# Kernel optimization log

Hardware: AMD Instinct MI355X
Metric: run time of the kernel (lower is better)

The kernel has to match this reference:

```python
import jax, jax.numpy as jnp
import numpy as np

B, H, W, C = 8, 64, 64, 256
CB = C // 2          # bottleneck_dim = channels // 2
COMPRESSION = 2      # max-pool factor on flattened spatial axis of phi and g


def setup_inputs() -> dict:
    key = jax.random.key(0)
    k = jax.random.split(key, 5)
    he = lambda kk, fan_in, shape: jax.random.normal(kk, shape, jnp.float32) * np.sqrt(2.0 / fan_in)
    return {
        "x": jax.random.normal(k[0], (B, H, W, C), jnp.float32),
        "W_theta": he(k[1], C, (C, CB)),
        "W_phi": he(k[2], C, (C, CB)),
        "W_g": he(k[3], C, (C, CB)),
        "W_out": he(k[4], CB, (CB, C)),
    }


def _maxpool1d(t, pool):
    # MaxPool1D(pool) along axis 1 of [B, N, C] (valid padding, stride=pool)
    b, n, c = t.shape
    return t.reshape(b, n // pool, pool, c).max(axis=2)


def reference(x, W_theta, W_phi, W_g, W_out):
    b, h, w, c = x.shape
    n = h * w
    xf = x.reshape(b, n, c)                      # flatten spatial dims
    theta = xf @ W_theta                         # [B, N, Cb] (1x1 conv, no bias)
    phi = _maxpool1d(xf @ W_phi, COMPRESSION)    # [B, N/2, Cb]
    g = _maxpool1d(xf @ W_g, COMPRESSION)        # [B, N/2, Cb]
    f = jax.nn.softmax(jnp.einsum('bnd,bmd->bnm', theta, phi), axis=-1)  # [B, N, N/2]
    y = jnp.einsum('bnm,bmd->bnd', f, g)         # [B, N, Cb]
    y = (y @ W_out).reshape(b, h, w, c)          # expand conv back to C
    return x + y                                 # add_residual=True
```

## Files before the change

### kernel.cpp

```cpp
#include <hip/hip_runtime.h>
#include <math.h>

#define BB 8
#define NN 4096
#define MM 2048
#define CC 256
#define CBD 128

typedef __attribute__((ext_vector_type(8))) short s16x8;
typedef __attribute__((ext_vector_type(8))) _Float16 f16x8;
typedef __attribute__((ext_vector_type(4))) float f32x4;
typedef __attribute__((ext_vector_type(16))) float f32x16;
typedef unsigned short u16;
typedef unsigned int u32;

__device__ __forceinline__ u16 f2bf(float f) {
    union { float f; u32 u; } v; v.f = f;
    u32 r = v.u + 0x7fffu + ((v.u >> 16) & 1u);
    return (u16)(r >> 16);
}
__device__ __forceinline__ float bf2f(u16 h) {
    union { u32 u; float f; } v; v.u = ((u32)h) << 16; return v.f;
}
__device__ __forceinline__ u16 f2h(float f) {
    union { _Float16 h; u16 u; } v; v.h = (_Float16)f; return v.u;
}
__device__ __forceinline__ u32 asu(float f) {
    union { float f; u32 u; } v; v.f = f; return v.u;
}
__device__ __forceinline__ u32 pkbf(float lo, float hi) {
    return __builtin_amdgcn_perm(asu(hi), asu(lo), 0x07060302u);
}

#define MFMA(a, b, c)    __builtin_amdgcn_mfma_f32_16x16x32_bf16(a, b, c, 0, 0, 0)
#define MFMAF(a, b, c)   __builtin_amdgcn_mfma_f32_16x16x32_f16(a, b, c, 0, 0, 0)
#define MFMA32(a, b, c)  __builtin_amdgcn_mfma_f32_32x32x16_bf16(a, b, c, 0, 0, 0)
#define MFMA32F(a, b, c) __builtin_amdgcn_mfma_f32_32x32x16_f16(a, b, c, 0, 0, 0)

__device__ __forceinline__ void gload_lds16(const u16* g, u16* l) {
    __builtin_amdgcn_global_load_lds(
        (const __attribute__((address_space(1))) void*)g,
        (__attribute__((address_space(3))) void*)l, 16, 0, 0);
}

__global__ __launch_bounds__(256) void k_split_w(
    const float* __restrict__ wt, const float* __restrict__ wp,
    const float* __restrict__ wg, const float* __restrict__ wo,
    u16* wtf, u16* wpf, u16* wgf, u16* wot) {
    int e = blockIdx.x * 256 + threadIdx.x;
    int m = blockIdx.y;
    if (m < 3) {
        const float* src = m == 0 ? wt : (m == 1 ? wp : wg);
        u16* of = m == 0 ? wtf : (m == 1 ? wpf : wgf);
        int r = e >> 7, c = e & 127;
        of[c * 256 + r] = f2h(src[e]);
    } else {
        int r = e >> 8, c = e & 255;
        wot[c * 128 + r] = f2bf(wo[e]);
    }
}

__global__ __launch_bounds__(256) void k_proj(
    const float* __restrict__ x,
    const u16* __restrict__ wtf, const u16* __restrict__ wpf,
    const u16* __restrict__ wgf,
    u16* __restrict__ th, u16* __restrict__ ph, u16* __restrict__ gt) {
    __shared__ u16 S[18176];
    const int THH = 0, PHH = 8704, GL = 13056;
    u16* sxf = S;
    u16* sw  = S + 2560;
    int tid = threadIdx.x;
    int w = tid >> 6, lane = tid & 63, q = lane >> 4, li = lane & 15;
    int r0 = blockIdx.x * 64;
    int wr2 = (w >> 1) * 32, wcc = (w & 1) * 64;
    const u16* Ws[3] = {wtf, wpf, wgf};

    f32x4 aT[2][4], aP[2][4], aG[2][4];
#pragma unroll
    for (int i = 0; i < 2; i++)
#pragma unroll
        for (int j = 0; j < 4; j++) {
            aT[i][j] = (f32x4)0.f; aP[i][j] = (f32x4)0.f; aG[i][j] = (f32x4)0.f;
        }

    for (int kc = 0; kc < 8; kc++) {
        {
            int row = tid >> 2, seg = tid & 3;
            const float* xp = &x[(size_t)(r0 + row) * 256 + kc * 32 + seg * 8];
            float4 v0 = ((const float4*)xp)[0];
            float4 v1 = ((const float4*)xp)[1];
            u16 hh[8];
            hh[0] = f2h(v0.x); hh[1] = f2h(v0.y);
            hh[2] = f2h(v0.z); hh[3] = f2h(v0.w);
            hh[4] = f2h(v1.x); hh[5] = f2h(v1.y);
            hh[6] = f2h(v1.z); hh[7] = f2h(v1.w);
            *(s16x8*)&sxf[row * 40 + seg * 8] = *(s16x8*)&hh[0];
        }
#pragma unroll
        for (int u = 0; u < 6; u++) {
            int mat = u >> 1;
            int col = (u & 1) * 64 + (tid >> 2), ch = tid & 3;
            s16x8 v = *(const s16x8*)&Ws[mat][(size_t)col * 256 + kc * 32 + ch * 8];
            *(s16x8*)&sw[mat * 5120 + col * 40 + ch * 8] = v;
        }
        __syncthreads();

        f16x8 af[2];
#pragma unroll
        for (int i = 0; i < 2; i++)
            af[i] = *(const f16x8*)&sxf[(wr2 + i * 16 + li) * 40 + q * 8];
#pragma unroll
        for (int j = 0; j < 4; j++) {
            int col = wcc + j * 16 + li;
            f16x8 bt = *(const f16x8*)&sw[0 * 5120 + col * 40 + q * 8];
            f16x8 bp = *(const f16x8*)&sw[1 * 5120 + col * 40 + q * 8];
            f16x8 bg = *(const f16x8*)&sw[2 * 5120 + col * 40 + q * 8];
#pragma unroll
            for (int i = 0; i < 2; i++) {
                aT[i][j] = MFMAF(af[i], bt, aT[i][j]);
                aP[i][j] = MFMAF(af[i], bp, aP[i][j]);
                aG[i][j] = MFMAF(af[i], bg, aG[i][j]);
            }
        }
        __syncthreads();
    }

#pragma unroll
    for (int i = 0; i < 2; i++)
#pragma unroll
        for (int j = 0; j < 4; j++) {
            int col = wcc + j * 16 + li;
#pragma unroll
            for (int reg = 0; reg < 4; reg++) {
                int row = wr2 + i * 16 + q * 4 + reg;
                S[THH + row * 136 + col] = f2h(aT[i][j][reg]);
            }
#pragma unroll
            for (int pr = 0; pr < 2; pr++) {
                int ml = (wr2 >> 1) + i * 8 + q * 2 + pr;
                float vp = fmaxf(aP[i][j][pr * 2], aP[i][j][pr * 2 + 1]);
                S[PHH + ml * 136 + col] = f2h(vp);
                float vg = fmaxf(aG[i][j][pr * 2], aG[i][j][pr * 2 + 1]);
                int ml2 = (ml & ~12) | ((ml & 4) << 1) | ((ml & 8) >> 1);
                S[GL + col * 40 + ml2] = f2bf(vg);
            }
        }
    __syncthreads();

#pragma unroll
    for (int p2 = 0; p2 < 4; p2++) {
        int u2 = tid + p2 * 256;
        int row = u2 >> 4, chk = u2 & 15;
        size_t gb = (size_t)(r0 + row) * 128 + chk * 8;
        *(s16x8*)&th[gb] = *(const s16x8*)&S[THH + row * 136 + chk * 8];
    }
    {
        int row = tid >> 3, chk = tid & 7;
        size_t gb = (size_t)((r0 >> 1) + row) * 128 + chk * 16;
        *(s16x8*)&ph[gb]     = *(const s16x8*)&S[PHH + row * 136 + chk * 16];
        *(s16x8*)&ph[gb + 8] = *(const s16x8*)&S[PHH + row * 136 + chk * 16 + 8];
    }
    {
        int col = tid >> 1, half = tid & 1;
        int b = r0 >> 12;
        int base = (r0 >> 1) & 2047;
        size_t gb = (size_t)b * (128 * 2048) + (size_t)col * 2048 + base + half * 16;
        *(s16x8*)&gt[gb]     = *(const s16x8*)&S[GL + col * 40 + half * 16];
        *(s16x8*)&gt[gb + 8] = *(const s16x8*)&S[GL + col * 40 + half * 16 + 8];
    }
}

__global__ __launch_bounds__(256, 2) void k_attn(
    const u16* __restrict__ th, const u16* __restrict__ ph,
    const u16* __restrict__ gt, u16* __restrict__ ot,
    float* __restrict__ Mv, float* __restrict__ Lv) {
    __shared__ u16 smem[17408];
    u16* skh = smem;
    u16* sg  = smem + 8192;
    int tid = threadIdx.x, w = tid >> 6, lane = tid & 63;
    int q = lane & 31, b = lane >> 5;
    int bb = blockIdx.y;
    int s = blockIdx.x & 1;
    int qt = blockIdx.x >> 1;
    int n0 = qt * 128;
    int row128 = w * 32 + q;
    size_t qrow = ((size_t)bb * 4096 + n0 + row128) * 128;

    f16x8 Qf[8];
#pragma unroll
    for (int ks = 0; ks < 8; ks++)
        Qf[ks] = *(const f16x8*)&th[qrow + ks * 16 + b * 8];

    float mrow = -INFINITY, lrow = 0.f;
    f32x16 o[4];
#pragma unroll
    for (int c = 0; c < 4; c++) o[c] = (f32x16)0.f;

    int r_hi = lane >> 4, c_hi = lane & 15;
    int r_lo = lane >> 3, c_lo = lane & 7;
    int k0 = s * 1024;

    for (int kt = 0; kt < 16; kt++) {
        int m0 = k0 + kt * 64;
        if (kt) __syncthreads();
#pragma unroll
        for (int jj = 0; jj < 4; jj++) {
            int r = w * 16 + jj * 4 + r_hi;
            int gc = c_hi ^ (r & 7);
            size_t ga = (((size_t)(bb * 2048 + m0 + r)) << 7) + gc * 8;
            gload_lds16(&ph[ga], &skh[(w * 16 + jj * 4) << 7]);
            int r2 = w * 32 + jj * 8 + r_lo;
            int gc2 = c_lo ^ (r2 & 7);
            size_t ga2 = (size_t)bb * (128 * 2048) + (size_t)r2 * 2048 + m0 + gc2 * 8;
            gload_lds16(&gt[ga2], &sg[(w * 32 + jj * 8) << 6]);
        }
        __syncthreads();

        f32x16 S[2];
        S[0] = (f32x16)0.f; S[1] = (f32x16)0.f;
        __builtin_amdgcn_s_setprio(1);
#pragma unroll
        for (int ks = 0; ks < 8; ks++) {
            int off0 = (q << 7) + (((ks * 2 + b) ^ (q & 7)) << 3);
            int r1 = 32 + q;
            int off1 = (r1 << 7) + (((ks * 2 + b) ^ (r1 & 7)) << 3);
            f16x8 a0 = *(const f16x8*)&skh[off0];
            f16x8 a1 = *(const f16x8*)&skh[off1];
            S[0] = MFMA32F(a0, Qf[ks], S[0]);
            S[1] = MFMA32F(a1, Qf[ks], S[1]);
        }
        __builtin_amdgcn_s_setprio(0);

        float t0[8];
#pragma unroll
        for (int r = 0; r < 8; r++)
            t0[r] = fmaxf(fmaxf(S[0][r], S[0][r + 8]),
                          fmaxf(S[1][r], S[1][r + 8]));
        float u0 = fmaxf(t0[0], t0[1]), u1 = fmaxf(t0[2], t0[3]);
        float u2 = fmaxf(t0[4], t0[5]), u3 = fmaxf(t0[6], t0[7]);
        float vmax = fmaxf(fmaxf(u0, u1), fmaxf(u2, u3));
        vmax = fmaxf(vmax, __shfl_xor(vmax, 32, 64));

        if (!__all(vmax - mrow <= 20.f)) {
            float nm = fmaxf(mrow, vmax);
            float alph = __expf(mrow - nm);
            mrow = nm;
            lrow *= alph;
#pragma unroll
            for (int c = 0; c < 4; c++)
#pragma unroll
                for (int r = 0; r < 16; r++) o[c][r] *= alph;
        }
        float rs0 = 0.f, rs1 = 0.f, rs2 = 0.f, rs3 = 0.f;
#pragma unroll
        for (int r = 0; r < 4; r++) {
            float p00 = __expf(S[0][r] - mrow);      S[0][r] = p00;      rs0 += p00;
            float p01 = __expf(S[0][r + 4] - mrow);  S[0][r + 4] = p01;  rs1 += p01;
            float p02 = __expf(S[0][r + 8] - mrow);  S[0][r + 8] = p02;  rs2 += p02;
            float p03 = __expf(S[0][r + 12] - mrow); S[0][r + 12] = p03; rs3 += p03;
            float p10 = __expf(S[1][r] - mrow);      S[1][r] = p10;      rs0 += p10;
            float p11 = __expf(S[1][r + 4] - mrow);  S[1][r + 4] = p11;  rs1 += p11;
            float p12 = __expf(S[1][r + 8] - mrow);  S[1][r + 8] = p12;  rs2 += p12;
            float p13 = __expf(S[1][r + 12] - mrow); S[1][r + 12] = p13; rs3 += p13;
        }
        float rs = (rs0 + rs1) + (rs2 + rs3);
        rs += __shfl_xor(rs, 32, 64);
        lrow += rs;

        __builtin_amdgcn_s_setprio(1);
#pragma unroll
        for (int t = 0; t < 4; t++) {
            int half = t >> 1, base = (t & 1) * 8;
            s16x8 Pf;
            u32* pf = (u32*)&Pf;
#pragma unroll
            for (int r2 = 0; r2 < 4; r2++)
                pf[r2] = pkbf(S[half][base + 2 * r2], S[half][base + 2 * r2 + 1]);
#pragma unroll
            for (int c = 0; c < 4; c++) {
                int ch = c * 32 + q;
                int off = (ch << 6) + (((t * 2 + b) ^ (ch & 7)) << 3);
                s16x8 gv = *(const s16x8*)&sg[off];
                o[c] = MFMA32(gv, Pf, o[c]);
            }
        }
        __builtin_amdgcn_s_setprio(0);
    }
    __syncthreads();

    u16* sc = smem;
#pragma unroll
    for (int c = 0; c < 4; c++)
#pragma unroll
        for (int r2 = 0; r2 < 8; r2++) {
            int ch = c * 32 + ((r2 & 1) << 1) + 8 * (r2 >> 1) + 4 * b;
            u32 pk = (u32)f2bf(o[c][2 * r2]) | ((u32)f2bf(o[c][2 * r2 + 1]) << 16);
            *(u32*)&sc[row128 * 136 + ch] = pk;
        }
    __syncthreads();
    size_t obase = ((size_t)s * 32768 + (size_t)bb * 4096 + n0) * 128;
    int rowy = tid >> 1;
#pragma unroll
    for (int j = 0; j < 8; j++) {
        int chk = (tid & 1) * 8 + j;
        s16x8 v = *(const s16x8*)&sc[rowy * 136 + chk * 8];
        *(s16x8*)&ot[obase + (size_t)rowy * 128 + chk * 8] = v;
    }
    if (b == 0) {
        int gi = s * 32768 + bb * 4096 + n0 + row128;
        Mv[gi] = mrow;
        Lv[gi] = lrow;
    }
}

__global__ __launch_bounds__(256) void k_out(
    const u16* __restrict__ ot, const float* __restrict__ Mv,
    const float* __restrict__ Lv, const u16* __restrict__ wot,
    const float* __restrict__ x, float* __restrict__ out) {
    __shared__ char lds_o[36864];
    u16 (*sy)[72] = (u16(*)[72])lds_o;
    u16 (*sw)[72] = (u16(*)[72])(lds_o + 18432);
    int tid = threadIdx.x, w = tid >> 6, lane = tid & 63, q = lane >> 4, li = lane & 15;
    int r0 = blockIdx.x * 128, c0 = blockIdx.y * 128;
    int wr = (w >> 1) * 64, wc = (w & 1) * 64;
    const size_t OS = (size_t)32768 * 128;

    float a1v[4], a2v[4];
#pragma unroll
    for (int i = 0; i < 4; i++) {
        int gr = r0 + ((tid + i * 256) >> 3);
        float m1 = Mv[gr], m2 = Mv[32768 + gr];
        float l1 = Lv[gr], l2 = Lv[32768 + gr];
        float Mx = fmaxf(m1, m2);
        float e1 = __expf(m1 - Mx), e2 = __expf(m2 - Mx);
        float inv = 1.f / (l1 * e1 + l2 * e2);
        a1v[i] = e1 * inv;
        a2v[i] = e2 * inv;
    }

    f32x4 acc[4][4];
#pragma unroll
    for (int i = 0; i < 4; i++)
#pragma unroll
        for (int j = 0; j < 4; j++) acc[i][j] = (f32x4)0.f;

    for (int kc = 0; kc < 2; kc++) {
#pragma unroll
        for (int i = 0; i < 4; i++) {
            int ch = tid + i * 256;
            int r = ch >> 3, cc = (ch & 7) * 8;
            size_t ga = (size_t)(r0 + r) * 128 + kc * 64 + cc;
            s16x8 o1 = *(const s16x8*)&ot[ga];
            s16x8 o2 = *(const s16x8*)&ot[OS + ga];
            s16x8 yv;
#pragma unroll
            for (int e = 0; e < 8; e++)
                yv[e] = (short)f2bf(bf2f((u16)o1[e]) * a1v[i] +
                                    bf2f((u16)o2[e]) * a2v[i]);
            *(s16x8*)&sy[r][cc] = yv;
            *(s16x8*)&sw[r][cc] = *(const s16x8*)&wot[(size_t)(c0 + r) * 128 + kc * 64 + cc];
        }
        __syncthreads();
#pragma unroll
        for (int ks = 0; ks < 2; ks++)
#pragma unroll
            for (int i = 0; i < 4; i++) {
                s16x8 a = *(const s16x8*)&sy[wr + i * 16 + li][ks * 32 + q * 8];
#pragma unroll
                for (int j = 0; j < 4; j++) {
                    s16x8 bv = *(const s16x8*)&sw[wc + j * 16 + li][ks * 32 + q * 8];
                    acc[i][j] = MFMA(a, bv, acc[i][j]);
                }
            }
        __syncthreads();
    }

    float* sT = (float*)lds_o;
#pragma unroll
    for (int h = 0; h < 2; h++) {
        __syncthreads();
        if ((w >> 1) == h) {
#pragma unroll
            for (int i = 0; i < 4; i++)
#pragma unroll
                for (int j = 0; j < 4; j++)
#pragma unroll
                    for (int reg = 0; reg < 4; reg++)
                        sT[(i * 16 + q * 4 + reg) * 132 + wc + j * 16 + li] =
                            acc[i][j][reg];
        }
        __syncthreads();
#pragma unroll
        for (int p = 0; p < 8; p++) {
            int r = (tid >> 5) + p * 8;
            int c4 = (tid & 31) * 4;
            f32x4 yv = *(f32x4*)&sT[r * 132 + c4];
            size_t row = (size_t)(r0 + h * 64 + r);
            float4 xv = *(const float4*)&x[row * 256 + c0 + c4];
            float4 ov;
            ov.x = xv.x + yv[0]; ov.y = xv.y + yv[1];
            ov.z = xv.z + yv[2]; ov.w = xv.w + yv[3];
            *(float4*)&out[row * 256 + c0 + c4] = ov;
        }
    }
}

extern "C" void kernel_launch(void* const* d_in, const int* in_sizes, int n_in,
                              void* d_out, int out_size, void* d_ws, size_t ws_size,
                              hipStream_t stream) {
    const float* x  = (const float*)d_in[0];
    const float* wt = (const float*)d_in[1];
    const float* wp = (const float*)d_in[2];
    const float* wg = (const float*)d_in[3];
    const float* wo = (const float*)d_in[4];
    float* out = (float*)d_out;

    char* p = (char*)d_ws;
    auto alloc = [&](size_t bytes) {
        char* r = p;
        p += (bytes + 255) & ~(size_t)255;
        return r;
    };
    const size_t NT = (size_t)BB * NN * CBD;
    const size_t NP = (size_t)BB * MM * CBD;

    u16* wtf = (u16*)alloc(CC * CBD * 2);
    u16* wpf = (u16*)alloc(CC * CBD * 2);
    u16* wgf = (u16*)alloc(CC * CBD * 2);
    u16* wot = (u16*)alloc(CC * CBD * 2);
    u16* th  = (u16*)alloc(NT * 2);
    u16* ph  = (u16*)alloc(NP * 2);
    u16* gt  = (u16*)alloc(NP * 2);
    float* Mv = (float*)alloc(2 * 32768 * 4);
    float* Lv = (float*)alloc(2 * 32768 * 4);
    u16* ot  = (u16*)alloc(2 * NT * 2);

    k_split_w<<<dim3(128, 4), 256, 0, stream>>>(wt, wp, wg, wo,
                                                wtf, wpf, wgf, wot);
    k_proj<<<dim3(512), 256, 0, stream>>>(x, wtf, wpf, wgf, th, ph, gt);
    k_attn<<<dim3(64, 8), 256, 0, stream>>>(th, ph, gt, ot, Mv, Lv);
    k_out<<<dim3(256, 2), 256, 0, stream>>>(ot, Mv, Lv, wot, x, out);
}
```

Measured before the change: 162.9 us.

## Prefetch projection tiles into registers and single-stage swizzled output GEMM

```diff
diff --git a/kernel.cpp b/kernel.cpp
--- a/kernel.cpp
+++ b/kernel.cpp
@@ -83,27 +83,41 @@
             aT[i][j] = (f32x4)0.f; aP[i][j] = (f32x4)0.f; aG[i][j] = (f32x4)0.f;
         }
 
+    int xrow = tid >> 2, xseg = tid & 3;
+    const float* xbase = &x[(size_t)(r0 + xrow) * 256 + xseg * 8];
+    int wcol = tid >> 2, wch = tid & 3;
+
+    float4 cx0 = ((const float4*)xbase)[0];
+    float4 cx1 = ((const float4*)xbase)[1];
+    s16x8 cw[6];
+#pragma unroll
+    for (int u = 0; u < 6; u++)
+        cw[u] = *(const s16x8*)&Ws[u >> 1][(size_t)((u & 1) * 64 + wcol) * 256 + wch * 8];
+
     for (int kc = 0; kc < 8; kc++) {
         {
-            int row = tid >> 2, seg = tid & 3;
-            const float* xp = &x[(size_t)(r0 + row) * 256 + kc * 32 + seg * 8];
-            float4 v0 = ((const float4*)xp)[0];
-            float4 v1 = ((const float4*)xp)[1];
             u16 hh[8];
-            hh[0] = f2h(v0.x); hh[1] = f2h(v0.y);
-            hh[2] = f2h(v0.z); hh[3] = f2h(v0.w);
-            hh[4] = f2h(v1.x); hh[5] = f2h(v1.y);
-            hh[6] = f2h(v1.z); hh[7] = f2h(v1.w);
-            *(s16x8*)&sxf[row * 40 + seg * 8] = *(s16x8*)&hh[0];
-        }
-#pragma unroll
-        for (int u = 0; u < 6; u++) {
-            int mat = u >> 1;
-            int col = (u & 1) * 64 + (tid >> 2), ch = tid & 3;
-            s16x8 v = *(const s16x8*)&Ws[mat][(size_t)col * 256 + kc * 32 + ch * 8];
-            *(s16x8*)&sw[mat * 5120 + col * 40 + ch * 8] = v;
+            hh[0] = f2h(cx0.x); hh[1] = f2h(cx0.y);
+            hh[2] = f2h(cx0.z); hh[3] = f2h(cx0.w);
+            hh[4] = f2h(cx1.x); hh[5] = f2h(cx1.y);
+            hh[6] = f2h(cx1.z); hh[7] = f2h(cx1.w);
+            *(s16x8*)&sxf[xrow * 40 + xseg * 8] = *(s16x8*)&hh[0];
+#pragma unroll
+            for (int u = 0; u < 6; u++)
+                *(s16x8*)&sw[(u >> 1) * 5120 + ((u & 1) * 64 + wcol) * 40 + wch * 8] = cw[u];
         }
         __syncthreads();
+
+        float4 nx0, nx1; s16x8 nw[6];
+        if (kc < 7) {
+            const float* xp = xbase + (kc + 1) * 32;
+            nx0 = ((const float4*)xp)[0];
+            nx1 = ((const float4*)xp)[1];
+#pragma unroll
+            for (int u = 0; u < 6; u++)
+                nw[u] = *(const s16x8*)&Ws[u >> 1][(size_t)((u & 1) * 64 + wcol) * 256 +
+                                                  (kc + 1) * 32 + wch * 8];
+        }
 
         f16x8 af[2];
 #pragma unroll
@@ -123,6 +137,11 @@
             }
         }
         __syncthreads();
+        if (kc < 7) {
+            cx0 = nx0; cx1 = nx1;
+#pragma unroll
+            for (int u = 0; u < 6; u++) cw[u] = nw[u];
+        }
     }
 
 #pragma unroll
@@ -317,18 +336,22 @@
     const u16* __restrict__ ot, const float* __restrict__ Mv,
     const float* __restrict__ Lv, const u16* __restrict__ wot,
     const float* __restrict__ x, float* __restrict__ out) {
-    __shared__ char lds_o[36864];
-    u16 (*sy)[72] = (u16(*)[72])lds_o;
-    u16 (*sw)[72] = (u16(*)[72])(lds_o + 18432);
+    __shared__ char lds_o[65536];
+    u16 (*sy)[128] = (u16(*)[128])lds_o;
+    u16 (*sw)[128] = (u16(*)[128])(lds_o + 32768);
     int tid = threadIdx.x, w = tid >> 6, lane = tid & 63, q = lane >> 4, li = lane & 15;
     int r0 = blockIdx.x * 128, c0 = blockIdx.y * 128;
     int wr = (w >> 1) * 64, wc = (w & 1) * 64;
     const size_t OS = (size_t)32768 * 128;
 
-    float a1v[4], a2v[4];
-#pragma unroll
-    for (int i = 0; i < 4; i++) {
-        int gr = r0 + ((tid + i * 256) >> 3);
+    int sr = tid >> 4;
+    int cc = (tid & 15) * 8;
+    int swc = tid & 15;
+
+    float a1v[8], a2v[8];
+#pragma unroll
+    for (int i = 0; i < 8; i++) {
+        int gr = r0 + sr + i * 16;
         float m1 = Mv[gr], m2 = Mv[32768 + gr];
         float l1 = Lv[gr], l2 = Lv[32768 + gr];
         float Mx = fmaxf(m1, m2);
@@ -338,41 +361,46 @@
         a2v[i] = e2 * inv;
     }
 
+#pragma unroll
+    for (int i = 0; i < 8; i++) {
+        int r = sr + i * 16;
+        size_t ga = (size_t)(r0 + r) * 128 + cc;
+        s16x8 o1 = *(const s16x8*)&ot[ga];
+        s16x8 o2 = *(const s16x8*)&ot[OS + ga];
+        u32 yv[4];
+#pragma unroll
+        for (int e = 0; e < 4; e++) {
+            float v0 = bf2f((u16)o1[2 * e])     * a1v[i] + bf2f((u16)o2[2 * e])     * a2v[i];
+            float v1 = bf2f((u16)o1[2 * e + 1]) * a1v[i] + bf2f((u16)o2[2 * e + 1]) * a2v[i];
+            yv[e] = pkbf(v0, v1);
+        }
+        int sc2 = (swc ^ (r & 7)) * 8;
+        *(s16x8*)&sy[r][sc2] = *(const s16x8*)&yv[0];
+        *(s16x8*)&sw[r][sc2] = *(const s16x8*)&wot[(size_t)(c0 + r) * 128 + cc];
+    }
+    __syncthreads();
+
     f32x4 acc[4][4];
 #pragma unroll
     for (int i = 0; i < 4; i++)
 #pragma unroll
         for (int j = 0; j < 4; j++) acc[i][j] = (f32x4)0.f;
 
-    for (int kc = 0; kc < 2; kc++) {
+#pragma unroll
+    for (int ks = 0; ks < 4; ks++) {
+        s16x8 av[4], bv[4];
 #pragma unroll
         for (int i = 0; i < 4; i++) {
-            int ch = tid + i * 256;
-            int r = ch >> 3, cc = (ch & 7) * 8;
-            size_t ga = (size_t)(r0 + r) * 128 + kc * 64 + cc;
-            s16x8 o1 = *(const s16x8*)&ot[ga];
-            s16x8 o2 = *(const s16x8*)&ot[OS + ga];
-            s16x8 yv;
-#pragma unroll
-            for (int e = 0; e < 8; e++)
-                yv[e] = (short)f2bf(bf2f((u16)o1[e]) * a1v[i] +
-                                    bf2f((u16)o2[e]) * a2v[i]);
-            *(s16x8*)&sy[r][cc] = yv;
-            *(s16x8*)&sw[r][cc] = *(const s16x8*)&wot[(size_t)(c0 + r) * 128 + kc * 64 + cc];
-        }
-        __syncthreads();
-#pragma unroll
-        for (int ks = 0; ks < 2; ks++)
-#pragma unroll
-            for (int i = 0; i < 4; i++) {
-                s16x8 a = *(const s16x8*)&sy[wr + i * 16 + li][ks * 32 + q * 8];
-#pragma unroll
-                for (int j = 0; j < 4; j++) {
-                    s16x8 bv = *(const s16x8*)&sw[wc + j * 16 + li][ks * 32 + q * 8];
-                    acc[i][j] = MFMA(a, bv, acc[i][j]);
-                }
-            }
-        __syncthreads();
+            int ar = wr + i * 16 + li;
+            av[i] = *(const s16x8*)&sy[ar][((ks * 4 + q) ^ (ar & 7)) * 8];
+            int br = wc + i * 16 + li;
+            bv[i] = *(const s16x8*)&sw[br][((ks * 4 + q) ^ (br & 7)) * 8];
+        }
+#pragma unroll
+        for (int i = 0; i < 4; i++)
+#pragma unroll
+            for (int j = 0; j < 4; j++)
+                acc[i][j] = MFMA(av[i], bv[j], acc[i][j]);
     }
 
     float* sT = (float*)lds_o;
```

After: 159.0 us. 2.4% less time.
